# Kernel optimization log

Measured on AMD Instinct MI355X. Metric: run time of the kernel, lower is better.

## Reference

```python
import jax, jax.numpy as jnp
import numpy as np

N_NODES = 100000
N_EDGES = 1000000
IN_DIM = 128
OUT_DIM = 64
NEG_SLOPE = 0.2


def setup_inputs() -> dict:
    key = jax.random.key(0)
    k = jax.random.split(key, 6)
    h = jax.random.normal(k[0], (N_NODES, IN_DIM), dtype=jnp.float32)
    # xavier-uniform-ish scales for linear weights
    W_w = jax.random.uniform(k[1], (OUT_DIM, IN_DIM), dtype=jnp.float32,
                             minval=-1.0, maxval=1.0) * np.sqrt(6.0 / (IN_DIM + OUT_DIM))
    W_b = jnp.zeros((OUT_DIM,), dtype=jnp.float32)
    a_w = jax.random.uniform(k[2], (1, 2 * OUT_DIM), dtype=jnp.float32,
                             minval=-1.0, maxval=1.0) * np.sqrt(6.0 / (2 * OUT_DIM + 1))
    a_b = jnp.zeros((1,), dtype=jnp.float32)
    edge_index = jax.random.randint(k[3], (2, N_EDGES), 0, N_NODES, dtype=jnp.int64)
    return {"h": h, "W_w": W_w, "W_b": W_b, "a_w": a_w, "a_b": a_b,
            "edge_index": edge_index}


def reference(h, W_w, W_b, a_w, a_b, edge_index):
    # Wh = W(h): [N, D_out]
    Wh = h @ W_w.T + W_b
    src, tgt = edge_index[0], edge_index[1]
    D = Wh.shape[1]
    # a([e_src, e_tgt]) decomposes: score = Wh@a_src per-node + Wh@a_tgt per-node,
    # gathered by edge (avoids materializing the [E, 2D] concat).
    s_src = Wh @ a_w[0, :D]   # [N]
    s_tgt = Wh @ a_w[0, D:]   # [N]
    logits = jax.nn.leaky_relu(s_src[src] + s_tgt[tgt] + a_b[0], NEG_SLOPE)  # [E]
    # NOTE: global softmax over all edges (dim=0), faithful to the source.
    attn = jax.nn.softmax(logits, axis=0)
    e_src = Wh[src]  # [E, D] gather
    messages = jnp.zeros_like(Wh).at[tgt].add(attn[:, None] * e_src)  # scatter-add
    return jax.nn.leaky_relu(messages, NEG_SLOPE)
```

## Files before the change

### kernel.cpp

```cpp
#include <hip/hip_runtime.h>
#include <math.h>

#define N_NODES 100000
#define N_EDGES 1000000
#define IN_DIM  128
#define OUT_DIM 64
#define NEG     0.2f

#define SCAN_BLOCKS 391
#define EDGE_BLOCKS 3907

#define G_GROUPS 32
#define EPG      (N_EDGES / G_GROUPS)
#define CHUNK_N  25000
#define HIST_BLOCKS (G_GROUPS * 4)

typedef __attribute__((ext_vector_type(8))) short short8;
typedef __attribute__((ext_vector_type(4))) float f32x4;

#define MFMA(A, B, C) __builtin_amdgcn_mfma_f32_16x16x32_bf16(A, B, C, 0, 0, 0)

union U16 { unsigned u[4]; short8 s; };

__device__ __forceinline__ void split8(const float* x, short8& hi, short8& lo) {
    U16 H, L;
#pragma unroll
    for (int i = 0; i < 4; ++i) {
        float a = x[2 * i], b = x[2 * i + 1];
        unsigned ua = __float_as_uint(a), ub = __float_as_uint(b);
        unsigned ha = ua & 0xffff0000u, hb = ub & 0xffff0000u;
        H.u[i] = (ua >> 16) | hb;
        float la = a - __uint_as_float(ha);
        float lb = b - __uint_as_float(hb);
        L.u[i] = (__float_as_uint(la) >> 16) | (__float_as_uint(lb) & 0xffff0000u);
    }
    hi = H.s; lo = L.s;
}

__device__ __forceinline__ unsigned pk2(float a, float b) {
    unsigned ua = __float_as_uint(a); ua = (ua + 0x7fffu + ((ua >> 16) & 1u)) >> 16;
    unsigned ub = __float_as_uint(b); ub = (ub + 0x7fffu + ((ub >> 16) & 1u)) >> 16;
    return ua | (ub << 16);
}

__global__ __launch_bounds__(256, 3) void k1_mfma(
    const float* __restrict__ h, const float* __restrict__ W,
    const float* __restrict__ Wb, const float* __restrict__ aw,
    unsigned short* __restrict__ Whb, float* __restrict__ s_src,
    float* __restrict__ s_tgt)
{
    __shared__ float4 smem4[2176];
    unsigned short* wfh = (unsigned short*)smem4;
    unsigned short* wfl = wfh + 8192;

    const int tid  = threadIdx.x;
    const int lane = tid & 63, w = tid >> 6;
    const int c = lane & 15, g = lane >> 4;
    const int n0 = blockIdx.x * 128;

#pragma unroll
    for (int it = 0; it < 4; ++it) {
        int U = tid + 256 * it;
        int pos = U >> 6, l = U & 63;
        int nb = pos >> 2, ks = pos & 3;
        int r  = 16 * nb + (l & 15);
        int k0 = 32 * ks + 8 * (l >> 4);
        float a[8];
        *(float4*)&a[0] = *(const float4*)(W + r * IN_DIM + k0);
        *(float4*)&a[4] = *(const float4*)(W + r * IN_DIM + k0 + 4);
        short8 hi, lo; split8(a, hi, lo);
        *(short8*)(wfh + (size_t)U * 8) = hi;
        *(short8*)(wfl + (size_t)U * 8) = lo;
    }
    __syncthreads();

    const int na0 = n0 + 32 * w + c;
    const float* hp0 = h + (size_t)min(na0, N_NODES - 1) * IN_DIM + 8 * g;
    const float* hp1 = h + (size_t)min(na0 + 16, N_NODES - 1) * IN_DIM + 8 * g;

    f32x4 acc[2][4];
    {
        f32x4 z = {0.f, 0.f, 0.f, 0.f};
#pragma unroll
        for (int m = 0; m < 2; ++m)
#pragma unroll
            for (int nb = 0; nb < 4; ++nb) acc[m][nb] = z;
    }

#pragma unroll 2
    for (int ks = 0; ks < 4; ++ks) {
        short8 bh[4], bl[4];
#pragma unroll
        for (int nb = 0; nb < 4; ++nb) {
            int u = ((nb * 4 + ks) * 64 + lane) * 8;
            bh[nb] = *(const short8*)(wfh + u);
            bl[nb] = *(const short8*)(wfl + u);
        }
        float am[8];
        short8 ah, al;
        *(float4*)&am[0] = *(const float4*)(hp0 + 32 * ks);
        *(float4*)&am[4] = *(const float4*)(hp0 + 32 * ks + 4);
        split8(am, ah, al);
#pragma unroll
        for (int nb = 0; nb < 4; ++nb) {
            acc[0][nb] = MFMA(ah, bh[nb], acc[0][nb]);
            acc[0][nb] = MFMA(ah, bl[nb], acc[0][nb]);
            acc[0][nb] = MFMA(al, bh[nb], acc[0][nb]);
        }
        *(float4*)&am[0] = *(const float4*)(hp1 + 32 * ks);
        *(float4*)&am[4] = *(const float4*)(hp1 + 32 * ks + 4);
        split8(am, ah, al);
#pragma unroll
        for (int nb = 0; nb < 4; ++nb) {
            acc[1][nb] = MFMA(ah, bh[nb], acc[1][nb]);
            acc[1][nb] = MFMA(ah, bl[nb], acc[1][nb]);
            acc[1][nb] = MFMA(al, bh[nb], acc[1][nb]);
        }
    }

    float wb[4], w1[4], w2[4];
#pragma unroll
    for (int nb = 0; nb < 4; ++nb) {
        wb[nb] = Wb[16 * nb + c];
        w1[nb] = aw[16 * nb + c];
        w2[nb] = aw[OUT_DIM + 16 * nb + c];
    }
#pragma unroll
    for (int m = 0; m < 2; ++m)
#pragma unroll
        for (int r = 0; r < 4; ++r) {
            float s1 = 0.f, s2 = 0.f;
#pragma unroll
            for (int nb = 0; nb < 4; ++nb) {
                float v = acc[m][nb][r] + wb[nb];
                acc[m][nb][r] = v;
                s1 = fmaf(v, w1[nb], s1);
                s2 = fmaf(v, w2[nb], s2);
            }
#pragma unroll
            for (int mk = 1; mk < 16; mk <<= 1) {
                s1 += __shfl_xor(s1, mk);
                s2 += __shfl_xor(s2, mk);
            }
            if (c == 0) {
                int node = n0 + 32 * w + 16 * m + 4 * g + r;
                if (node < N_NODES) { s_src[node] = s1; s_tgt[node] = s2; }
            }
        }

    __syncthreads();
    float* tr = (float*)smem4;
#pragma unroll
    for (int m = 0; m < 2; ++m)
#pragma unroll
        for (int nb = 0; nb < 4; ++nb)
#pragma unroll
            for (int r = 0; r < 4; ++r)
                tr[(32 * w + 16 * m + 4 * g + r) * 68 + 16 * nb + c] = acc[m][nb][r];
    __syncthreads();

#pragma unroll
    for (int j = 0; j < 4; ++j) {
        int idx = tid + 256 * j;
        int nloc = idx >> 3, q = idx & 7;
        int node = n0 + nloc;
        if (node < N_NODES) {
            const float* r8 = &tr[nloc * 68 + q * 8];
            uint4 u;
            u.x = pk2(r8[0], r8[1]); u.y = pk2(r8[2], r8[3]);
            u.z = pk2(r8[4], r8[5]); u.w = pk2(r8[6], r8[7]);
            ((uint4*)Whb)[(size_t)node * 8 + q] = u;
        }
    }
}

__global__ __launch_bounds__(256) void k_hist(
    const int* __restrict__ ei, unsigned char* __restrict__ deg_g8,
    unsigned* __restrict__ rank)
{
    __shared__ unsigned cnt[CHUNK_N];
    const int g  = blockIdx.x >> 2;
    const int c0 = (blockIdx.x & 3) * CHUNK_N;
    const int tid = threadIdx.x;

    for (int i = tid; i < CHUNK_N; i += 256) cnt[i] = 0u;
    __syncthreads();

    const int ebase = g * EPG;
    const int2* tp2 = (const int2*)(ei + N_EDGES + ebase);
#pragma unroll 4
    for (int i = tid; i < EPG / 2; i += 256) {
        int2 tv = tp2[i];
        int e0 = ebase + 2 * i;
        unsigned u0 = (unsigned)(tv.x - c0), u1 = (unsigned)(tv.y - c0);
        if (u0 < CHUNK_N) rank[e0]     = atomicAdd(&cnt[u0], 1u);
        if (u1 < CHUNK_N) rank[e0 + 1] = atomicAdd(&cnt[u1], 1u);
    }
    __syncthreads();

    unsigned* dg = (unsigned*)(deg_g8 + (size_t)g * N_NODES + c0);
    for (int i = tid; i < CHUNK_N / 4; i += 256) {
        unsigned v = cnt[4 * i] | (cnt[4 * i + 1] << 8) |
                     (cnt[4 * i + 2] << 16) | (cnt[4 * i + 3] << 24);
        dg[i] = v;
    }
}

__global__ __launch_bounds__(256) void k_scanA(
    const unsigned char* __restrict__ deg_g8, unsigned* __restrict__ psum)
{
    const int i = blockIdx.x * 256 + threadIdx.x;
    unsigned v = 0;
    if (i < N_NODES) {
#pragma unroll
        for (int x = 0; x < G_GROUPS; ++x)
            v += deg_g8[(size_t)x * N_NODES + i];
    }
#pragma unroll
    for (int off = 32; off; off >>= 1) v += __shfl_xor(v, off);
    __shared__ unsigned us[4];
    if ((threadIdx.x & 63) == 0) us[threadIdx.x >> 6] = v;
    __syncthreads();
    if (threadIdx.x == 0) psum[blockIdx.x] = us[0] + us[1] + us[2] + us[3];
}

__global__ __launch_bounds__(256) void k_scan3(
    const unsigned char* __restrict__ deg_g8, const unsigned* __restrict__ psum,
    unsigned* __restrict__ row, unsigned* __restrict__ row_g)
{
    __shared__ unsigned sc[256];
    __shared__ unsigned ps[4];
    const int t = threadIdx.x;
    const int i = blockIdx.x * 256 + t;

    unsigned pv = 0;
    if (t < blockIdx.x) pv = psum[t];
    if (t + 256 < blockIdx.x) pv += psum[t + 256];
#pragma unroll
    for (int off = 32; off; off >>= 1) pv += __shfl_xor(pv, off);
    if ((t & 63) == 0) ps[t >> 6] = pv;

    unsigned d[G_GROUPS];
    unsigned tot = 0;
    if (i < N_NODES) {
#pragma unroll
        for (int x = 0; x < G_GROUPS; ++x) {
            d[x] = deg_g8[(size_t)x * N_NODES + i];
            tot += d[x];
        }
    }
    sc[t] = tot;
    __syncthreads();
    for (int off = 1; off < 256; off <<= 1) {
        unsigned u = (t >= off) ? sc[t - off] : 0u;
        __syncthreads();
        sc[t] += u;
        __syncthreads();
    }
    const unsigned bb = ps[0] + ps[1] + ps[2] + ps[3];
    if (i < N_NODES) {
        unsigned base = bb + sc[t] - tot;
        row[i] = base;
        unsigned run = base;
#pragma unroll
        for (int x = 0; x < G_GROUPS; ++x) {
            row_g[(size_t)x * N_NODES + i] = run;
            run += d[x];
        }
    }
    if (i == 0) row[N_NODES] = N_EDGES;
}

__global__ __launch_bounds__(256) void k_fill(
    const int* __restrict__ ei, const float* __restrict__ s_src,
    const float* __restrict__ s_tgt, const float* __restrict__ ab,
    const unsigned* __restrict__ rank, const unsigned* __restrict__ row_g,
    int2* __restrict__ bin, float* __restrict__ bsum)
{
    const float ab0 = ab[0];
    float lsum = 0.f;
    const int e = blockIdx.x * 256 + threadIdx.x;
    if (e < N_EDGES) {
        int s = ei[e], t = ei[N_EDGES + e];
        float x = s_src[s] + s_tgt[t] + ab0;
        float l = x > 0.f ? x : NEG * x;
        float ex = __expf(l);
        lsum = ex;
        int g = e / EPG;
        unsigned pos = row_g[(size_t)g * N_NODES + t] + rank[e];
        bin[pos] = make_int2(s, __float_as_int(ex));
    }
#pragma unroll
    for (int off = 32; off; off >>= 1) lsum += __shfl_xor(lsum, off);
    __shared__ float ssum[4];
    if ((threadIdx.x & 63) == 0) ssum[threadIdx.x >> 6] = lsum;
    __syncthreads();
    if (threadIdx.x == 0)
        bsum[blockIdx.x] = ssum[0] + ssum[1] + ssum[2] + ssum[3];
}

__global__ __launch_bounds__(512) void k_gsum(
    const float* __restrict__ bsum, float* __restrict__ gsum)
{
    __shared__ float sf[8];
    const int t = threadIdx.x;
    float s = 0.f;
    for (int i = t; i < EDGE_BLOCKS; i += 512) s += bsum[i];
#pragma unroll
    for (int off = 32; off; off >>= 1) s += __shfl_xor(s, off);
    if ((t & 63) == 0) sf[t >> 6] = s;
    __syncthreads();
    if (t == 0) {
        float tot = 0.f;
#pragma unroll
        for (int i = 0; i < 8; ++i) tot += sf[i];
        gsum[0] = tot;
    }
}

__global__ __launch_bounds__(256) void k_gather(
    const unsigned* __restrict__ row, const int2* __restrict__ bin,
    const float* __restrict__ gsum, const unsigned short* __restrict__ Whb,
    float* __restrict__ out)
{
    const int lane = threadIdx.x & 63;
    const int tb = blockIdx.x * 16 + (threadIdx.x >> 6) * 4;
    const int q = lane >> 4, sub = lane & 15;

    const unsigned r0 = row[tb],     r1 = row[tb + 1], r2 = row[tb + 2];
    const unsigned r3 = row[tb + 3], r4 = row[tb + 4];
    unsigned base0 = r0, base1 = r1, base2 = r2, base3 = r3;

    f32x4 a0 = {0.f, 0.f, 0.f, 0.f}, a1 = a0, a2 = a0, a3 = a0;

    while (base0 < r1 || base1 < r2 || base2 < r3 || base3 < r4) {
        const int c0 = base0 < r1 ? (int)min(64u, r1 - base0) : 0;
        const int c1 = base1 < r2 ? (int)min(64u, r2 - base1) : 0;
        const int c2 = base2 < r3 ? (int)min(64u, r3 - base2) : 0;
        const int c3 = base3 < r4 ? (int)min(64u, r4 - base3) : 0;
        int2 p0 = make_int2(0, 0), p1 = p0, p2 = p0, p3 = p0;
        if (lane < c0) p0 = bin[base0 + lane];
        if (lane < c1) p1 = bin[base1 + lane];
        if (lane < c2) p2 = bin[base2 + lane];
        if (lane < c3) p3 = bin[base3 + lane];
        const int cm = max(max(c0, c1), max(c2, c3));
        for (int j = 0; j < cm; j += 4) {
            int   s0 = __shfl(p0.x, j + q);
            float w0 = __int_as_float(__shfl(p0.y, j + q));
            int   s1 = __shfl(p1.x, j + q);
            float w1 = __int_as_float(__shfl(p1.y, j + q));
            int   s2 = __shfl(p2.x, j + q);
            float w2 = __int_as_float(__shfl(p2.y, j + q));
            int   s3 = __shfl(p3.x, j + q);
            float w3 = __int_as_float(__shfl(p3.y, j + q));
            ushort4 v0 = *(const ushort4*)(Whb + (size_t)s0 * OUT_DIM + 4 * sub);
            ushort4 v1 = *(const ushort4*)(Whb + (size_t)s1 * OUT_DIM + 4 * sub);
            ushort4 v2 = *(const ushort4*)(Whb + (size_t)s2 * OUT_DIM + 4 * sub);
            ushort4 v3 = *(const ushort4*)(Whb + (size_t)s3 * OUT_DIM + 4 * sub);
            a0.x = fmaf(w0, __uint_as_float((unsigned)v0.x << 16), a0.x);
            a0.y = fmaf(w0, __uint_as_float((unsigned)v0.y << 16), a0.y);
            a0.z = fmaf(w0, __uint_as_float((unsigned)v0.z << 16), a0.z);
            a0.w = fmaf(w0, __uint_as_float((unsigned)v0.w << 16), a0.w);
            a1.x = fmaf(w1, __uint_as_float((unsigned)v1.x << 16), a1.x);
            a1.y = fmaf(w1, __uint_as_float((unsigned)v1.y << 16), a1.y);
            a1.z = fmaf(w1, __uint_as_float((unsigned)v1.z << 16), a1.z);
            a1.w = fmaf(w1, __uint_as_float((unsigned)v1.w << 16), a1.w);
            a2.x = fmaf(w2, __uint_as_float((unsigned)v2.x << 16), a2.x);
            a2.y = fmaf(w2, __uint_as_float((unsigned)v2.y << 16), a2.y);
            a2.z = fmaf(w2, __uint_as_float((unsigned)v2.z << 16), a2.z);
            a2.w = fmaf(w2, __uint_as_float((unsigned)v2.w << 16), a2.w);
            a3.x = fmaf(w3, __uint_as_float((unsigned)v3.x << 16), a3.x);
            a3.y = fmaf(w3, __uint_as_float((unsigned)v3.y << 16), a3.y);
            a3.z = fmaf(w3, __uint_as_float((unsigned)v3.z << 16), a3.z);
            a3.w = fmaf(w3, __uint_as_float((unsigned)v3.w << 16), a3.w);
        }
        base0 += 64; base1 += 64; base2 += 64; base3 += 64;
    }

    const float inv = 1.0f / gsum[0];
#pragma unroll
    for (int n = 0; n < 4; ++n) {
        f32x4 a = (n == 0) ? a0 : (n == 1) ? a1 : (n == 2) ? a2 : a3;
        a.x += __shfl_xor(a.x, 16); a.x += __shfl_xor(a.x, 32);
        a.y += __shfl_xor(a.y, 16); a.y += __shfl_xor(a.y, 32);
        a.z += __shfl_xor(a.z, 16); a.z += __shfl_xor(a.z, 32);
        a.w += __shfl_xor(a.w, 16); a.w += __shfl_xor(a.w, 32);
        float r = (q == 0) ? a.x : (q == 1) ? a.y : (q == 2) ? a.z : a.w;
        r *= inv;
        r = r > 0.f ? r : NEG * r;
        out[(size_t)(tb + n) * OUT_DIM + 4 * sub + q] = r;
    }
}

extern "C" void kernel_launch(void* const* d_in, const int* in_sizes, int n_in,
                              void* d_out, int out_size, void* d_ws, size_t ws_size,
                              hipStream_t stream)
{
    const float* h  = (const float*)d_in[0];
    const float* W  = (const float*)d_in[1];
    const float* Wb = (const float*)d_in[2];
    const float* aw = (const float*)d_in[3];
    const float* ab = (const float*)d_in[4];
    const int*   ei = (const int*)d_in[5];

    unsigned short* Whb = (unsigned short*)d_ws;
    int2*  bin   = (int2*)(Whb + (size_t)N_NODES * OUT_DIM);
    float* s_src = (float*)(bin + N_EDGES);
    float* s_tgt = s_src + N_NODES;
    unsigned char* deg_g8 = (unsigned char*)(s_tgt + N_NODES);
    unsigned* row   = (unsigned*)(deg_g8 + (size_t)G_GROUPS * N_NODES);
    unsigned* row_g = row + N_NODES + 1;
    unsigned* psum  = row_g + (size_t)G_GROUPS * N_NODES;
    unsigned* rank  = psum + 512;
    float* bsum  = (float*)(rank + N_EDGES);
    float* gsum  = bsum + 4096;

    float* out = (float*)d_out;

    k_hist<<<HIST_BLOCKS, 256, 0, stream>>>(ei, deg_g8, rank);
    k1_mfma<<<(N_NODES + 127) / 128, 256, 0, stream>>>(h, W, Wb, aw, Whb,
                                                       s_src, s_tgt);
    k_scanA<<<SCAN_BLOCKS, 256, 0, stream>>>(deg_g8, psum);
    k_scan3<<<SCAN_BLOCKS, 256, 0, stream>>>(deg_g8, psum, row, row_g);
    k_fill<<<EDGE_BLOCKS, 256, 0, stream>>>(ei, s_src, s_tgt, ab, rank,
                                            row_g, bin, bsum);
    k_gsum<<<1, 512, 0, stream>>>(bsum, gsum);
    k_gather<<<(N_NODES + 15) / 16, 256, 0, stream>>>(row, bin, gsum, Whb, out);
}
```

Before: 204.0 us.

## Pack histogram counters to 16-bit in LDS and raise edge group count

The histogram kernel now packs two 16-bit counters per 32-bit LDS word, halving shared memory per block so more blocks fit per CU. The edge-group count rises from 32 to 80, giving more histogram blocks with fewer edges each, and loads are batched eight at a time to raise memory-level parallelism. The scan kernel stops holding the per-group degrees in registers and re-reads them from memory to avoid register pressure with 80 groups. In exchange, the extra groups increase deg_g8 and row_g traffic in the scan kernels, and the 8-bit per-group degree limit still holds.

New measurement: 203.0 us. No clear change (-0.5%).

```diff
diff --git a/kernel.cpp b/kernel.cpp
--- a/kernel.cpp
+++ b/kernel.cpp
@@ -10,8 +10,9 @@
 #define SCAN_BLOCKS 391
 #define EDGE_BLOCKS 3907
 
-#define G_GROUPS 32
+#define G_GROUPS 80
 #define EPG      (N_EDGES / G_GROUPS)
+#define NI2      (EPG / 2)
 #define CHUNK_N  25000
 #define HIST_BLOCKS (G_GROUPS * 4)
 
@@ -178,31 +179,47 @@
     const int* __restrict__ ei, unsigned char* __restrict__ deg_g8,
     unsigned* __restrict__ rank)
 {
-    __shared__ unsigned cnt[CHUNK_N];
+    __shared__ unsigned cnt[CHUNK_N / 2];
     const int g  = blockIdx.x >> 2;
     const int c0 = (blockIdx.x & 3) * CHUNK_N;
     const int tid = threadIdx.x;
 
-    for (int i = tid; i < CHUNK_N; i += 256) cnt[i] = 0u;
+    for (int i = tid; i < CHUNK_N / 2; i += 256) cnt[i] = 0u;
     __syncthreads();
 
     const int ebase = g * EPG;
     const int2* tp2 = (const int2*)(ei + N_EDGES + ebase);
-#pragma unroll 4
-    for (int i = tid; i < EPG / 2; i += 256) {
-        int2 tv = tp2[i];
-        int e0 = ebase + 2 * i;
-        unsigned u0 = (unsigned)(tv.x - c0), u1 = (unsigned)(tv.y - c0);
-        if (u0 < CHUNK_N) rank[e0]     = atomicAdd(&cnt[u0], 1u);
-        if (u1 < CHUNK_N) rank[e0 + 1] = atomicAdd(&cnt[u1], 1u);
+    for (int b = 0; b < 32; b += 8) {
+        int2 tv[8];
+#pragma unroll
+        for (int k = 0; k < 8; ++k) {
+            int idx = tid + (b + k) * 256;
+            tv[k] = (idx < NI2) ? tp2[idx] : make_int2(-0x40000000, -0x40000000);
+        }
+#pragma unroll
+        for (int k = 0; k < 8; ++k) {
+            int idx = tid + (b + k) * 256;
+            int e0 = ebase + 2 * idx;
+            unsigned u0 = (unsigned)(tv[k].x - c0), u1 = (unsigned)(tv[k].y - c0);
+            if (u0 < CHUNK_N) {
+                unsigned sh = (u0 & 1u) * 16u;
+                unsigned old = atomicAdd(&cnt[u0 >> 1], 1u << sh);
+                rank[e0] = (old >> sh) & 0xffffu;
+            }
+            if (u1 < CHUNK_N) {
+                unsigned sh = (u1 & 1u) * 16u;
+                unsigned old = atomicAdd(&cnt[u1 >> 1], 1u << sh);
+                rank[e0 + 1] = (old >> sh) & 0xffffu;
+            }
+        }
     }
     __syncthreads();
 
     unsigned* dg = (unsigned*)(deg_g8 + (size_t)g * N_NODES + c0);
     for (int i = tid; i < CHUNK_N / 4; i += 256) {
-        unsigned v = cnt[4 * i] | (cnt[4 * i + 1] << 8) |
-                     (cnt[4 * i + 2] << 16) | (cnt[4 * i + 3] << 24);
-        dg[i] = v;
+        unsigned w0 = cnt[2 * i], w1 = cnt[2 * i + 1];
+        dg[i] = (w0 & 0xffu) | (((w0 >> 16) & 0xffu) << 8) |
+                ((w1 & 0xffu) << 16) | (((w1 >> 16) & 0xffu) << 24);
     }
 }
 
@@ -240,14 +257,11 @@
     for (int off = 32; off; off >>= 1) pv += __shfl_xor(pv, off);
     if ((t & 63) == 0) ps[t >> 6] = pv;
 
-    unsigned d[G_GROUPS];
     unsigned tot = 0;
     if (i < N_NODES) {
 #pragma unroll
-        for (int x = 0; x < G_GROUPS; ++x) {
-            d[x] = deg_g8[(size_t)x * N_NODES + i];
-            tot += d[x];
-        }
+        for (int x = 0; x < G_GROUPS; ++x)
+            tot += deg_g8[(size_t)x * N_NODES + i];
     }
     sc[t] = tot;
     __syncthreads();
@@ -265,7 +279,7 @@
 #pragma unroll
         for (int x = 0; x < G_GROUPS; ++x) {
             row_g[(size_t)x * N_NODES + i] = run;
-            run += d[x];
+            run += deg_g8[(size_t)x * N_NODES + i];
         }
     }
     if (i == 0) row[N_NODES] = N_EDGES;
```
